# Optimization experiments

Hardware: AMD Instinct MI355X
Metric: run time of the kernel (lower is better)

Reference implementation:

```python
import jax, jax.numpy as jnp
import numpy as np

INPUT, HIDDEN, C, H, W, PK = 64, 128, 16, 32, 32, 4
B, T = 512, 1024

def hardsigmoid(v):
    return jnp.clip(v / 6.0 + 0.5, 0.0, 1.0)

def setup_inputs() -> dict:
    key = jax.random.key(0)
    ks = jax.random.split(key, 9)
    s_rnn = 1.0 / np.sqrt(HIDDEN)
    s_map = 1.0 / np.sqrt(HIDDEN)
    return {
        "x": jax.random.normal(ks[0], (B, T, INPUT), dtype=jnp.float32),
        "W_ih": jax.random.uniform(ks[1], (HIDDEN, INPUT), minval=-s_rnn, maxval=s_rnn),
        "b_ih": jax.random.uniform(ks[2], (HIDDEN,), minval=-s_rnn, maxval=s_rnn),
        "W_hh": jax.random.uniform(ks[3], (HIDDEN, HIDDEN), minval=-s_rnn, maxval=s_rnn),
        "b_hh": jax.random.uniform(ks[4], (HIDDEN,), minval=-s_rnn, maxval=s_rnn),
        "W_gate": jax.random.uniform(ks[5], (HIDDEN, HIDDEN), minval=-s_rnn, maxval=s_rnn),
        "b_gate": jax.random.uniform(ks[6], (HIDDEN,), minval=-s_rnn, maxval=s_rnn),
        "W_map": jax.random.uniform(ks[7], (C * H * W, HIDDEN), minval=-s_map, maxval=s_map),
        "b_map": jax.random.uniform(ks[8], (C * H * W,), minval=-s_map, maxval=s_map),
    }

def reference(x, W_ih, b_ih, W_hh, b_hh, W_gate, b_gate, W_map, b_map):
    batch, seq_len, _ = x.shape
    h0 = jnp.zeros((batch, HIDDEN), dtype=x.dtype)
    agg0 = jnp.zeros((batch, HIDDEN), dtype=x.dtype)

    def step(carry, xt):
        h, agg = carry
        h = jnp.tanh(xt @ W_ih.T + b_ih + h @ W_hh.T + b_hh)
        gate = hardsigmoid(h @ W_gate.T + b_gate)
        return (h, agg + h * gate), None

    (h, agg), _ = jax.lax.scan(step, (h0, agg0), jnp.swapaxes(x, 0, 1))
    agg = agg / float(seq_len)

    mapped = (agg @ W_map.T + b_map).reshape(batch, C, H, W)
    # AvgPool2d(kernel=PK, stride=PK) via reshape-mean
    pooled = mapped.reshape(batch, C, H // PK, PK, W // PK, PK).mean(axis=(3, 5))
    upsampled = jnp.repeat(jnp.repeat(pooled, PK, axis=2), PK, axis=3)
    return mapped * hardsigmoid(upsampled)
```

## Files before the change

kernel.cpp:

```cpp
#include <hip/hip_runtime.h>
#include <hip/hip_bf16.h>

#define T_SEQ 1024
#define BATCH 512
#define INPUT 64
#define HID   128

typedef __attribute__((ext_vector_type(8))) short bf16x8;
typedef __attribute__((ext_vector_type(4))) short s16x4;
typedef __attribute__((ext_vector_type(4))) float f32x4;
typedef __attribute__((ext_vector_type(2))) unsigned int u32x2;

#define MFMA __builtin_amdgcn_mfma_f32_16x16x32_bf16

__device__ __forceinline__ short f2bf(float f) {
    union { float f; unsigned u; } v; v.f = f;
    unsigned r = (v.u + 0x7FFFu + ((v.u >> 16) & 1u)) >> 16;
    return (short)r;
}

__device__ __forceinline__ unsigned cvtpk_bf16(float lo, float hi) {
    unsigned r;
    asm("v_cvt_pk_bf16_f32 %0, %1, %2" : "=v"(r) : "v"(lo), "v"(hi));
    return r;
}

__device__ __forceinline__ float fast_tanh(float s) {
    float e = __expf(2.0f * s);
    return 1.0f - 2.0f * __builtin_amdgcn_rcpf(e + 1.0f);
}

__device__ __forceinline__ float hsig(float v) {
    return __builtin_amdgcn_fmed3f(v * 0.16666666666666666f + 0.5f, 0.0f, 1.0f);
}

__device__ __forceinline__ void wg_barrier_lds() {
    asm volatile("s_waitcnt lgkmcnt(0)" ::: "memory");
    __builtin_amdgcn_s_barrier();
    asm volatile("" ::: "memory");
}

__global__ __launch_bounds__(256) void cvt_kernel(const float* __restrict__ in,
                                                  short* __restrict__ out, int n4) {
    int i = blockIdx.x * 256 + threadIdx.x;
    if (i >= n4) return;
    f32x4 v = ((const f32x4*)in)[i];
    s16x4 o;
    #pragma unroll
    for (int j = 0; j < 4; ++j) o[j] = f2bf(v[j]);
    ((s16x4*)out)[i] = o;
}

template<bool PRE>
__global__ __launch_bounds__(256) void rnn_kernel(
    const float* __restrict__ xf_, const short* __restrict__ xb,
    const float* __restrict__ W_ih, const float* __restrict__ b_ih,
    const float* __restrict__ W_hh, const float* __restrict__ b_hh,
    const float* __restrict__ W_gate, const float* __restrict__ b_gate,
    float* __restrict__ agg_out)
{
    __shared__ __align__(16) short sh[2][16][136];

    const int tid  = threadIdx.x;
    const int wave = tid >> 6, lane = tid & 63;
    const int q = lane >> 4, l15 = lane & 15;
    const int b0 = blockIdx.x * 16;
    const int R0 = 32 * wave, R1 = R0 + 16;

    bf16x8 wih[2][2], whh[2][4], wgf[2][4];
    #pragma unroll
    for (int tile = 0; tile < 2; ++tile) {
        const int row = (tile ? R1 : R0) + l15;
        #pragma unroll
        for (int f = 0; f < 2; ++f) {
            const float* p = W_ih + row * INPUT + f * 32 + q * 8;
            bf16x8 v;
            #pragma unroll
            for (int j = 0; j < 8; ++j) v[j] = f2bf(p[j]);
            wih[tile][f] = v;
        }
        #pragma unroll
        for (int f = 0; f < 4; ++f) {
            const float* p = W_hh + row * HID + f * 32 + q * 8;
            bf16x8 v;
            #pragma unroll
            for (int j = 0; j < 8; ++j) v[j] = f2bf(p[j]);
            whh[tile][f] = v;
        }
        #pragma unroll
        for (int f = 0; f < 4; ++f) {
            const float* p = W_gate + row * HID + f * 32 + q * 8;
            bf16x8 v;
            #pragma unroll
            for (int j = 0; j < 8; ++j) v[j] = f2bf(p[j]);
            wgf[tile][f] = v;
        }
    }

    f32x4 bias1[2], biasg[2], zero4;
    #pragma unroll
    for (int tile = 0; tile < 2; ++tile) {
        const int rbase = (tile ? R1 : R0) + q * 4;
        #pragma unroll
        for (int r = 0; r < 4; ++r) {
            bias1[tile][r] = b_ih[rbase + r] + b_hh[rbase + r];
            biasg[tile][r] = b_gate[rbase + r];
        }
    }
    #pragma unroll
    for (int r = 0; r < 4; ++r) zero4[r] = 0.0f;

    f32x4 agg0 = zero4, agg1 = zero4;
    f32x4 hp1_0 = zero4, hp1_1 = zero4;
    f32x4 hp2_0 = zero4, hp2_1 = zero4;
    f32x4 gat0 = zero4, gat1 = zero4;
    f32x4 axA0, axA1, axB0, axB1;
    bf16x8 xB0a, xB0b, xB1a, xB1b;

    const long lanebase = ((long)(b0 + l15) * T_SEQ) * INPUT + q * 8;
    const short* xb_lane = PRE ? (xb + lanebase) : nullptr;
    const float* xf_lane = PRE ? nullptr : (xf_ + lanebase);

    auto load_pair = [&](int tt, bf16x8& fa, bf16x8& fb) {
        if constexpr (PRE) {
            const short* p = xb_lane + (long)tt * INPUT;
            fa = *(const bf16x8*)p;
            fb = *(const bf16x8*)(p + 32);
        } else {
            const float* p = xf_lane + (long)tt * INPUT;
            f32x4 a0 = *(const f32x4*)p,        a1 = *(const f32x4*)(p + 4);
            f32x4 a2 = *(const f32x4*)(p + 32), a3 = *(const f32x4*)(p + 36);
            #pragma unroll
            for (int j = 0; j < 4; ++j) {
                fa[j] = f2bf(a0[j]); fa[4 + j] = f2bf(a1[j]);
                fb[j] = f2bf(a2[j]); fb[4 + j] = f2bf(a3[j]);
            }
        }
    };

    auto step = [&](int t, f32x4& axM0, f32x4& axM1, f32x4& axS0, f32x4& axS1,
                    bf16x8& xfa, bf16x8& xfb) {
        const int rb = (t & 1) ^ 1, wb = t & 1;
        bf16x8 hf0 = *(const bf16x8*)&sh[rb][l15][q * 8];
        bf16x8 hf1 = *(const bf16x8*)&sh[rb][l15][32 + q * 8];
        bf16x8 hf2 = *(const bf16x8*)&sh[rb][l15][64 + q * 8];
        bf16x8 hf3 = *(const bf16x8*)&sh[rb][l15][96 + q * 8];
        #pragma unroll
        for (int r = 0; r < 4; ++r) {
            agg0[r] += hp2_0[r] * hsig(gat0[r]);
            agg1[r] += hp2_1[r] * hsig(gat1[r]);
        }
        axS0 = MFMA(wih[0][0], xfa, bias1[0], 0, 0, 0);
        axS1 = MFMA(wih[1][0], xfa, bias1[1], 0, 0, 0);
        axS0 = MFMA(wih[0][1], xfb, axS0, 0, 0, 0);
        axS1 = MFMA(wih[1][1], xfb, axS1, 0, 0, 0);
        int tt = t + 3; if (tt > T_SEQ - 1) tt = T_SEQ - 1;
        load_pair(tt, xfa, xfb);
        f32x4 a0 = MFMA(whh[0][0], hf0, axM0, 0, 0, 0);
        f32x4 c0 = MFMA(whh[0][2], hf2, zero4, 0, 0, 0);
        f32x4 a1 = MFMA(whh[1][0], hf0, axM1, 0, 0, 0);
        f32x4 c1 = MFMA(whh[1][2], hf2, zero4, 0, 0, 0);
        a0 = MFMA(whh[0][1], hf1, a0, 0, 0, 0);
        c0 = MFMA(whh[0][3], hf3, c0, 0, 0, 0);
        a1 = MFMA(whh[1][1], hf1, a1, 0, 0, 0);
        c1 = MFMA(whh[1][3], hf3, c1, 0, 0, 0);
        gat0 = MFMA(wgf[0][0], hf0, biasg[0], 0, 0, 0);
        gat0 = MFMA(wgf[0][1], hf1, gat0, 0, 0, 0);
        gat0 = MFMA(wgf[0][2], hf2, gat0, 0, 0, 0);
        gat0 = MFMA(wgf[0][3], hf3, gat0, 0, 0, 0);
        gat1 = MFMA(wgf[1][0], hf0, biasg[1], 0, 0, 0);
        gat1 = MFMA(wgf[1][1], hf1, gat1, 0, 0, 0);
        gat1 = MFMA(wgf[1][2], hf2, gat1, 0, 0, 0);
        gat1 = MFMA(wgf[1][3], hf3, gat1, 0, 0, 0);
        hp2_0 = hp1_0; hp2_1 = hp1_1;
        hp1_0[0] = fast_tanh(a0[0] + c0[0]);
        hp1_0[1] = fast_tanh(a0[1] + c0[1]);
        hp1_0[2] = fast_tanh(a0[2] + c0[2]);
        hp1_0[3] = fast_tanh(a0[3] + c0[3]);
        hp1_1[0] = fast_tanh(a1[0] + c1[0]);
        hp1_1[1] = fast_tanh(a1[1] + c1[1]);
        hp1_1[2] = fast_tanh(a1[2] + c1[2]);
        hp1_1[3] = fast_tanh(a1[3] + c1[3]);
        u32x2 p0, p1;
        p0[0] = cvtpk_bf16(hp1_0[0], hp1_0[1]); p0[1] = cvtpk_bf16(hp1_0[2], hp1_0[3]);
        p1[0] = cvtpk_bf16(hp1_1[0], hp1_1[1]); p1[1] = cvtpk_bf16(hp1_1[2], hp1_1[3]);
        *(u32x2*)&sh[wb][l15][R0 + q * 4] = p0;
        *(u32x2*)&sh[wb][l15][R1 + q * 4] = p1;
        wg_barrier_lds();
    };

    {
        bf16x8 ta, tb;
        load_pair(0, ta, tb);
        axA0 = MFMA(wih[0][0], ta, bias1[0], 0, 0, 0);
        axA1 = MFMA(wih[1][0], ta, bias1[1], 0, 0, 0);
        axA0 = MFMA(wih[0][1], tb, axA0, 0, 0, 0);
        axA1 = MFMA(wih[1][1], tb, axA1, 0, 0, 0);
        hp1_0[0] = fast_tanh(axA0[0]); hp1_0[1] = fast_tanh(axA0[1]);
        hp1_0[2] = fast_tanh(axA0[2]); hp1_0[3] = fast_tanh(axA0[3]);
        hp1_1[0] = fast_tanh(axA1[0]); hp1_1[1] = fast_tanh(axA1[1]);
        hp1_1[2] = fast_tanh(axA1[2]); hp1_1[3] = fast_tanh(axA1[3]);
        u32x2 p0, p1;
        p0[0] = cvtpk_bf16(hp1_0[0], hp1_0[1]); p0[1] = cvtpk_bf16(hp1_0[2], hp1_0[3]);
        p1[0] = cvtpk_bf16(hp1_1[0], hp1_1[1]); p1[1] = cvtpk_bf16(hp1_1[2], hp1_1[3]);
        *(u32x2*)&sh[0][l15][R0 + q * 4] = p0;
        *(u32x2*)&sh[0][l15][R1 + q * 4] = p1;
        load_pair(1, ta, tb);
        axA0 = MFMA(wih[0][0], ta, bias1[0], 0, 0, 0);
        axA1 = MFMA(wih[1][0], ta, bias1[1], 0, 0, 0);
        axA0 = MFMA(wih[0][1], tb, axA0, 0, 0, 0);
        axA1 = MFMA(wih[1][1], tb, axA1, 0, 0, 0);
        load_pair(2, xB0a, xB0b);
        load_pair(3, xB1a, xB1b);
        wg_barrier_lds();
    }

    for (int i = 0; i < 511; ++i) {
        step(2 * i + 1, axA0, axA1, axB0, axB1, xB0a, xB0b);
        step(2 * i + 2, axB0, axB1, axA0, axA1, xB1a, xB1b);
    }
    step(1023, axA0, axA1, axB0, axB1, xB0a, xB0b);

    #pragma unroll
    for (int r = 0; r < 4; ++r) {
        agg0[r] += hp2_0[r] * hsig(gat0[r]);
        agg1[r] += hp2_1[r] * hsig(gat1[r]);
    }
    {
        bf16x8 hf0 = *(const bf16x8*)&sh[1][l15][q * 8];
        bf16x8 hf1 = *(const bf16x8*)&sh[1][l15][32 + q * 8];
        bf16x8 hf2 = *(const bf16x8*)&sh[1][l15][64 + q * 8];
        bf16x8 hf3 = *(const bf16x8*)&sh[1][l15][96 + q * 8];
        gat0 = MFMA(wgf[0][0], hf0, biasg[0], 0, 0, 0);
        gat0 = MFMA(wgf[0][1], hf1, gat0, 0, 0, 0);
        gat0 = MFMA(wgf[0][2], hf2, gat0, 0, 0, 0);
        gat0 = MFMA(wgf[0][3], hf3, gat0, 0, 0, 0);
        gat1 = MFMA(wgf[1][0], hf0, biasg[1], 0, 0, 0);
        gat1 = MFMA(wgf[1][1], hf1, gat1, 0, 0, 0);
        gat1 = MFMA(wgf[1][2], hf2, gat1, 0, 0, 0);
        gat1 = MFMA(wgf[1][3], hf3, gat1, 0, 0, 0);
        #pragma unroll
        for (int r = 0; r < 4; ++r) {
            agg0[r] += hp1_0[r] * hsig(gat0[r]);
            agg1[r] += hp1_1[r] * hsig(gat1[r]);
        }
    }
    const float s = 1.0f / (float)T_SEQ;
    #pragma unroll
    for (int r = 0; r < 4; ++r) { agg0[r] *= s; agg1[r] *= s; }
    *(f32x4*)&agg_out[(long)(b0 + l15) * HID + R0 + q * 4] = agg0;
    *(f32x4*)&agg_out[(long)(b0 + l15) * HID + R1 + q * 4] = agg1;
}

template<bool PRE>
__global__ __launch_bounds__(256) void map_kernel(
    const float* __restrict__ agg, const float* __restrict__ Wf,
    const short* __restrict__ Wb, const float* __restrict__ b_map,
    float* __restrict__ mapped)
{
    const int tid  = threadIdx.x;
    const int wave = tid >> 6, lane = tid & 63;
    const int q = lane >> 4, l15 = lane & 15;
    const int mb = blockIdx.x & 31;
    const int nb = blockIdx.x >> 5;
    const int b0 = mb * 16;
    const int n0 = nb * 128 + wave * 32;

    bf16x8 af[4];
    #pragma unroll
    for (int kb = 0; kb < 4; ++kb) {
        const float* p = agg + (b0 + l15) * HID + kb * 32 + q * 8;
        bf16x8 f;
        #pragma unroll
        for (int j = 0; j < 8; ++j) f[j] = f2bf(p[j]);
        af[kb] = f;
    }
    #pragma unroll
    for (int tn = 0; tn < 2; ++tn) {
        int nn = n0 + tn * 16 + l15;
        float bias = b_map[nn];
        f32x4 c;
        #pragma unroll
        for (int r = 0; r < 4; ++r) c[r] = bias;
        #pragma unroll
        for (int kb = 0; kb < 4; ++kb) {
            bf16x8 f;
            if (PRE) {
                f = *(const bf16x8*)(Wb + (long)nn * HID + kb * 32 + q * 8);
            } else {
                const float* p = Wf + (long)nn * HID + kb * 32 + q * 8;
                #pragma unroll
                for (int j = 0; j < 8; ++j) f[j] = f2bf(p[j]);
            }
            c = __builtin_amdgcn_mfma_f32_16x16x32_bf16(af[kb], f, c, 0, 0, 0);
        }
        #pragma unroll
        for (int r = 0; r < 4; ++r)
            mapped[(long)(b0 + q * 4 + r) * 16384 + nn] = c[r];
    }
}

__global__ __launch_bounds__(256) void pool_gate_kernel(float* __restrict__ mapped)
{
    __shared__ float sh_part[256];
    __shared__ float sh_gate[64];
    const int tid = threadIdx.x;
    float* plane = mapped + (long)blockIdx.x * 1024;

    f32x4 m4 = *(const f32x4*)(plane + tid * 4);
    sh_part[tid] = m4[0] + m4[1] + m4[2] + m4[3];
    __syncthreads();
    if (tid < 64) {
        int ph = tid >> 3, pw = tid & 7;
        float s = 0.0f;
        #pragma unroll
        for (int i = 0; i < 4; ++i) s += sh_part[(4 * ph + i) * 8 + pw];
        sh_gate[tid] = hsig(s * (1.0f / 16.0f));
    }
    __syncthreads();
    int h = tid >> 3, wb = tid & 7;
    float g = sh_gate[(h >> 2) * 8 + wb];
    f32x4 o = m4 * g;
    *(f32x4*)(plane + tid * 4) = o;
}

extern "C" void kernel_launch(void* const* d_in, const int* in_sizes, int n_in,
                              void* d_out, int out_size, void* d_ws, size_t ws_size,
                              hipStream_t stream) {
    const float* x      = (const float*)d_in[0];
    const float* W_ih   = (const float*)d_in[1];
    const float* b_ih   = (const float*)d_in[2];
    const float* W_hh   = (const float*)d_in[3];
    const float* b_hh   = (const float*)d_in[4];
    const float* W_gate = (const float*)d_in[5];
    const float* b_gate = (const float*)d_in[6];
    const float* W_map  = (const float*)d_in[7];
    const float* b_map  = (const float*)d_in[8];
    float* out = (float*)d_out;

    const size_t xb_bytes = (size_t)BATCH * T_SEQ * INPUT * 2;
    const size_t wm_bytes = (size_t)16384 * HID * 2;
    const size_t agg_bytes = (size_t)BATCH * HID * 4;
    const bool pre = ws_size >= xb_bytes + wm_bytes + agg_bytes;

    if (pre) {
        short* x_bf  = (short*)d_ws;
        short* wm_bf = (short*)((char*)d_ws + xb_bytes);
        float* agg   = (float*)((char*)d_ws + xb_bytes + wm_bytes);

        cvt_kernel<<<(BATCH * T_SEQ * INPUT / 4 + 255) / 256, 256, 0, stream>>>(x, x_bf, BATCH * T_SEQ * INPUT / 4);
        cvt_kernel<<<(16384 * HID / 4 + 255) / 256, 256, 0, stream>>>(W_map, wm_bf, 16384 * HID / 4);
        rnn_kernel<true><<<32, 256, 0, stream>>>(x, x_bf, W_ih, b_ih, W_hh, b_hh,
                                                 W_gate, b_gate, agg);
        map_kernel<true><<<4096, 256, 0, stream>>>(agg, W_map, wm_bf, b_map, out);
    } else {
        float* agg = (float*)d_ws;
        rnn_kernel<false><<<32, 256, 0, stream>>>(x, nullptr, W_ih, b_ih, W_hh, b_hh,
                                                  W_gate, b_gate, agg);
        map_kernel<false><<<4096, 256, 0, stream>>>(agg, W_map, nullptr, b_map, out);
    }
    pool_gate_kernel<<<BATCH * 16, 256, 0, stream>>>(out);
}
```

Measured before the change: 718.4 us.

## Split RNN batch across twice as many blocks with 8 rows each

The recurrent kernel now gives each workgroup 8 batch rows instead of 16 and launches 64 blocks instead of 32. This spreads the serial time loop over more compute units. The MFMA tiles still cover 16 columns, so lanes 8-15 duplicate rows 0-7 and only the first 8 lanes write results, which wastes half the matrix work. The gate accumulation is also moved to use gate values from the current step instead of ones carried from the previous iteration, which removes the hp2/gat registers but puts the hardsigmoid on the per-step critical path.

```diff
diff --git a/kernel.cpp b/kernel.cpp
--- a/kernel.cpp
+++ b/kernel.cpp
@@ -64,7 +64,8 @@
     const int tid  = threadIdx.x;
     const int wave = tid >> 6, lane = tid & 63;
     const int q = lane >> 4, l15 = lane & 15;
-    const int b0 = blockIdx.x * 16;
+    const int b0 = blockIdx.x * 8;
+    const int xbatch = b0 + (l15 & 7);
     const int R0 = 32 * wave, R1 = R0 + 16;
 
     bf16x8 wih[2][2], whh[2][4], wgf[2][4];
@@ -111,13 +112,11 @@
     for (int r = 0; r < 4; ++r) zero4[r] = 0.0f;
 
     f32x4 agg0 = zero4, agg1 = zero4;
-    f32x4 hp1_0 = zero4, hp1_1 = zero4;
-    f32x4 hp2_0 = zero4, hp2_1 = zero4;
-    f32x4 gat0 = zero4, gat1 = zero4;
+    f32x4 hp0 = zero4, hp1 = zero4;
     f32x4 axA0, axA1, axB0, axB1;
     bf16x8 xB0a, xB0b, xB1a, xB1b;
 
-    const long lanebase = ((long)(b0 + l15) * T_SEQ) * INPUT + q * 8;
+    const long lanebase = ((long)xbatch * T_SEQ) * INPUT + q * 8;
     const short* xb_lane = PRE ? (xb + lanebase) : nullptr;
     const float* xf_lane = PRE ? nullptr : (xf_ + lanebase);
 
@@ -145,11 +144,6 @@
         bf16x8 hf1 = *(const bf16x8*)&sh[rb][l15][32 + q * 8];
         bf16x8 hf2 = *(const bf16x8*)&sh[rb][l15][64 + q * 8];
         bf16x8 hf3 = *(const bf16x8*)&sh[rb][l15][96 + q * 8];
-        #pragma unroll
-        for (int r = 0; r < 4; ++r) {
-            agg0[r] += hp2_0[r] * hsig(gat0[r]);
-            agg1[r] += hp2_1[r] * hsig(gat1[r]);
-        }
         axS0 = MFMA(wih[0][0], xfa, bias1[0], 0, 0, 0);
         axS1 = MFMA(wih[1][0], xfa, bias1[1], 0, 0, 0);
         axS0 = MFMA(wih[0][1], xfb, axS0, 0, 0, 0);
@@ -164,26 +158,32 @@
         c0 = MFMA(whh[0][3], hf3, c0, 0, 0, 0);
         a1 = MFMA(whh[1][1], hf1, a1, 0, 0, 0);
         c1 = MFMA(whh[1][3], hf3, c1, 0, 0, 0);
-        gat0 = MFMA(wgf[0][0], hf0, biasg[0], 0, 0, 0);
-        gat0 = MFMA(wgf[0][1], hf1, gat0, 0, 0, 0);
-        gat0 = MFMA(wgf[0][2], hf2, gat0, 0, 0, 0);
-        gat0 = MFMA(wgf[0][3], hf3, gat0, 0, 0, 0);
-        gat1 = MFMA(wgf[1][0], hf0, biasg[1], 0, 0, 0);
-        gat1 = MFMA(wgf[1][1], hf1, gat1, 0, 0, 0);
-        gat1 = MFMA(wgf[1][2], hf2, gat1, 0, 0, 0);
-        gat1 = MFMA(wgf[1][3], hf3, gat1, 0, 0, 0);
-        hp2_0 = hp1_0; hp2_1 = hp1_1;
-        hp1_0[0] = fast_tanh(a0[0] + c0[0]);
-        hp1_0[1] = fast_tanh(a0[1] + c0[1]);
-        hp1_0[2] = fast_tanh(a0[2] + c0[2]);
-        hp1_0[3] = fast_tanh(a0[3] + c0[3]);
-        hp1_1[0] = fast_tanh(a1[0] + c1[0]);
-        hp1_1[1] = fast_tanh(a1[1] + c1[1]);
-        hp1_1[2] = fast_tanh(a1[2] + c1[2]);
-        hp1_1[3] = fast_tanh(a1[3] + c1[3]);
+        f32x4 g0 = MFMA(wgf[0][0], hf0, biasg[0], 0, 0, 0);
+        g0 = MFMA(wgf[0][1], hf1, g0, 0, 0, 0);
+        g0 = MFMA(wgf[0][2], hf2, g0, 0, 0, 0);
+        g0 = MFMA(wgf[0][3], hf3, g0, 0, 0, 0);
+        f32x4 g1 = MFMA(wgf[1][0], hf0, biasg[1], 0, 0, 0);
+        g1 = MFMA(wgf[1][1], hf1, g1, 0, 0, 0);
+        g1 = MFMA(wgf[1][2], hf2, g1, 0, 0, 0);
+        g1 = MFMA(wgf[1][3], hf3, g1, 0, 0, 0);
+        float t00 = fast_tanh(a0[0] + c0[0]);
+        float t01 = fast_tanh(a0[1] + c0[1]);
+        float t02 = fast_tanh(a0[2] + c0[2]);
+        float t03 = fast_tanh(a0[3] + c0[3]);
+        float t10 = fast_tanh(a1[0] + c1[0]);
+        float t11 = fast_tanh(a1[1] + c1[1]);
+        float t12 = fast_tanh(a1[2] + c1[2]);
+        float t13 = fast_tanh(a1[3] + c1[3]);
+        #pragma unroll
+        for (int r = 0; r < 4; ++r) {
+            agg0[r] += hp0[r] * hsig(g0[r]);
+            agg1[r] += hp1[r] * hsig(g1[r]);
+        }
+        hp0[0] = t00; hp0[1] = t01; hp0[2] = t02; hp0[3] = t03;
+        hp1[0] = t10; hp1[1] = t11; hp1[2] = t12; hp1[3] = t13;
         u32x2 p0, p1;
-        p0[0] = cvtpk_bf16(hp1_0[0], hp1_0[1]); p0[1] = cvtpk_bf16(hp1_0[2], hp1_0[3]);
-        p1[0] = cvtpk_bf16(hp1_1[0], hp1_1[1]); p1[1] = cvtpk_bf16(hp1_1[2], hp1_1[3]);
+        p0[0] = cvtpk_bf16(t00, t01); p0[1] = cvtpk_bf16(t02, t03);
+        p1[0] = cvtpk_bf16(t10, t11); p1[1] = cvtpk_bf16(t12, t13);
         *(u32x2*)&sh[wb][l15][R0 + q * 4] = p0;
         *(u32x2*)&sh[wb][l15][R1 + q * 4] = p1;
         wg_barrier_lds();
@@ -196,13 +196,13 @@
         axA1 = MFMA(wih[1][0], ta, bias1[1], 0, 0, 0);
         axA0 = MFMA(wih[0][1], tb, axA0, 0, 0, 0);
         axA1 = MFMA(wih[1][1], tb, axA1, 0, 0, 0);
-        hp1_0[0] = fast_tanh(axA0[0]); hp1_0[1] = fast_tanh(axA0[1]);
-        hp1_0[2] = fast_tanh(axA0[2]); hp1_0[3] = fast_tanh(axA0[3]);
-        hp1_1[0] = fast_tanh(axA1[0]); hp1_1[1] = fast_tanh(axA1[1]);
-        hp1_1[2] = fast_tanh(axA1[2]); hp1_1[3] = fast_tanh(axA1[3]);
+        hp0[0] = fast_tanh(axA0[0]); hp0[1] = fast_tanh(axA0[1]);
+        hp0[2] = fast_tanh(axA0[2]); hp0[3] = fast_tanh(axA0[3]);
+        hp1[0] = fast_tanh(axA1[0]); hp1[1] = fast_tanh(axA1[1]);
+        hp1[2] = fast_tanh(axA1[2]); hp1[3] = fast_tanh(axA1[3]);
         u32x2 p0, p1;
-        p0[0] = cvtpk_bf16(hp1_0[0], hp1_0[1]); p0[1] = cvtpk_bf16(hp1_0[2], hp1_0[3]);
-        p1[0] = cvtpk_bf16(hp1_1[0], hp1_1[1]); p1[1] = cvtpk_bf16(hp1_1[2], hp1_1[3]);
+        p0[0] = cvtpk_bf16(hp0[0], hp0[1]); p0[1] = cvtpk_bf16(hp0[2], hp0[3]);
+        p1[0] = cvtpk_bf16(hp1[0], hp1[1]); p1[1] = cvtpk_bf16(hp1[2], hp1[3]);
         *(u32x2*)&sh[0][l15][R0 + q * 4] = p0;
         *(u32x2*)&sh[0][l15][R1 + q * 4] = p1;
         load_pair(1, ta, tb);
@@ -221,35 +221,32 @@
     }
     step(1023, axA0, axA1, axB0, axB1, xB0a, xB0b);
 
-    #pragma unroll
-    for (int r = 0; r < 4; ++r) {
-        agg0[r] += hp2_0[r] * hsig(gat0[r]);
-        agg1[r] += hp2_1[r] * hsig(gat1[r]);
-    }
     {
         bf16x8 hf0 = *(const bf16x8*)&sh[1][l15][q * 8];
         bf16x8 hf1 = *(const bf16x8*)&sh[1][l15][32 + q * 8];
         bf16x8 hf2 = *(const bf16x8*)&sh[1][l15][64 + q * 8];
         bf16x8 hf3 = *(const bf16x8*)&sh[1][l15][96 + q * 8];
-        gat0 = MFMA(wgf[0][0], hf0, biasg[0], 0, 0, 0);
-        gat0 = MFMA(wgf[0][1], hf1, gat0, 0, 0, 0);
-        gat0 = MFMA(wgf[0][2], hf2, gat0, 0, 0, 0);
-        gat0 = MFMA(wgf[0][3], hf3, gat0, 0, 0, 0);
-        gat1 = MFMA(wgf[1][0], hf0, biasg[1], 0, 0, 0);
-        gat1 = MFMA(wgf[1][1], hf1, gat1, 0, 0, 0);
-        gat1 = MFMA(wgf[1][2], hf2, gat1, 0, 0, 0);
-        gat1 = MFMA(wgf[1][3], hf3, gat1, 0, 0, 0);
+        f32x4 g0 = MFMA(wgf[0][0], hf0, biasg[0], 0, 0, 0);
+        g0 = MFMA(wgf[0][1], hf1, g0, 0, 0, 0);
+        g0 = MFMA(wgf[0][2], hf2, g0, 0, 0, 0);
+        g0 = MFMA(wgf[0][3], hf3, g0, 0, 0, 0);
+        f32x4 g1 = MFMA(wgf[1][0], hf0, biasg[1], 0, 0, 0);
+        g1 = MFMA(wgf[1][1], hf1, g1, 0, 0, 0);
+        g1 = MFMA(wgf[1][2], hf2, g1, 0, 0, 0);
+        g1 = MFMA(wgf[1][3], hf3, g1, 0, 0, 0);
         #pragma unroll
         for (int r = 0; r < 4; ++r) {
-            agg0[r] += hp1_0[r] * hsig(gat0[r]);
-            agg1[r] += hp1_1[r] * hsig(gat1[r]);
-        }
-    }
-    const float s = 1.0f / (float)T_SEQ;
-    #pragma unroll
-    for (int r = 0; r < 4; ++r) { agg0[r] *= s; agg1[r] *= s; }
-    *(f32x4*)&agg_out[(long)(b0 + l15) * HID + R0 + q * 4] = agg0;
-    *(f32x4*)&agg_out[(long)(b0 + l15) * HID + R1 + q * 4] = agg1;
+            agg0[r] += hp0[r] * hsig(g0[r]);
+            agg1[r] += hp1[r] * hsig(g1[r]);
+        }
+    }
+    if (l15 < 8) {
+        const float s = 1.0f / (float)T_SEQ;
+        #pragma unroll
+        for (int r = 0; r < 4; ++r) { agg0[r] *= s; agg1[r] *= s; }
+        *(f32x4*)&agg_out[(long)(b0 + l15) * HID + R0 + q * 4] = agg0;
+        *(f32x4*)&agg_out[(long)(b0 + l15) * HID + R1 + q * 4] = agg1;
+    }
 }
 
 template<bool PRE>
@@ -350,12 +347,12 @@
 
         cvt_kernel<<<(BATCH * T_SEQ * INPUT / 4 + 255) / 256, 256, 0, stream>>>(x, x_bf, BATCH * T_SEQ * INPUT / 4);
         cvt_kernel<<<(16384 * HID / 4 + 255) / 256, 256, 0, stream>>>(W_map, wm_bf, 16384 * HID / 4);
-        rnn_kernel<true><<<32, 256, 0, stream>>>(x, x_bf, W_ih, b_ih, W_hh, b_hh,
+        rnn_kernel<true><<<64, 256, 0, stream>>>(x, x_bf, W_ih, b_ih, W_hh, b_hh,
                                                  W_gate, b_gate, agg);
         map_kernel<true><<<4096, 256, 0, stream>>>(agg, W_map, wm_bf, b_map, out);
     } else {
         float* agg = (float*)d_ws;
-        rnn_kernel<false><<<32, 256, 0, stream>>>(x, nullptr, W_ih, b_ih, W_hh, b_hh,
+        rnn_kernel<false><<<64, 256, 0, stream>>>(x, nullptr, W_ih, b_ih, W_hh, b_hh,
                                                   W_gate, b_gate, agg);
         map_kernel<false><<<4096, 256, 0, stream>>>(agg, W_map, nullptr, b_map, out);
     }
```

New measurement: 707.3 us. About the same (-1.5%).
